# Performance work log

Hardware: AMD Instinct MI355X
Metric: run time of the kernel (lower is better)

Reference implementation:

```python
import jax, jax.numpy as jnp
import numpy as np

D_MODEL = 1024
NUM_HEADS = 16
HEAD_DIM = D_MODEL // NUM_HEADS
THETA = 10000.0
B, T = 4, 2048


def _cos_sin(seq_len, head_dim, theta):
    # [T, head_dim]: first half cos, second half sin (matches precompute_freqs_cis)
    freqs = 1.0 / theta ** (jnp.arange(0, head_dim, 2, dtype=jnp.float32) / head_dim)
    t = jnp.arange(seq_len, dtype=jnp.float32)
    angles = jnp.outer(t, freqs)  # [T, head_dim//2]
    return jnp.concatenate([jnp.cos(angles), jnp.sin(angles)], axis=-1)


def _apply_rope(x, cos_sin):
    # x: [B, H, T, Hd]; even/odd interleaved pairs rotated
    x1 = x[..., 0::2]
    x2 = x[..., 1::2]
    half = x.shape[-1] // 2
    cos = cos_sin[:, :half]  # [T, Hd//2]
    sin = cos_sin[:, half:]
    out = jnp.stack([x1 * cos - x2 * sin, x1 * sin + x2 * cos], axis=-1)
    return out.reshape(x.shape)


def setup_inputs() -> dict:
    key = jax.random.key(0)
    k1, k2, k3 = jax.random.split(key, 3)
    x = jax.random.normal(k1, (B, T, D_MODEL), dtype=jnp.float32)
    W_qkv = jax.random.normal(k2, (3 * D_MODEL, D_MODEL), dtype=jnp.float32) * (D_MODEL ** -0.5)
    W_out = jax.random.normal(k3, (D_MODEL, D_MODEL), dtype=jnp.float32) * (D_MODEL ** -0.5)
    return {"x": x, "W_qkv": W_qkv, "W_out": W_out}


def reference(x, W_qkv, W_out):
    Bsz, Tlen, _ = x.shape
    # fused QKV projection: einsum('...i,oi->...o')
    qkv = jnp.einsum('bti,oi->bto', x, W_qkv)  # [B, T, 3*d_model]
    # 'B T (nH Hs) -> B nH T Hs' with nH = 3*num_heads, then chunk along heads
    qkv = qkv.reshape(Bsz, Tlen, 3 * NUM_HEADS, HEAD_DIM).transpose(0, 2, 1, 3)
    q, k, v = jnp.split(qkv, 3, axis=1)  # each [B, nH, T, Hd]
    cos_sin = _cos_sin(Tlen, HEAD_DIM, THETA)
    q = _apply_rope(q, cos_sin)
    k = _apply_rope(k, cos_sin)
    scores = jnp.einsum('bhqd,bhkd->bhqk', q, k) / np.sqrt(HEAD_DIM).astype(np.float32)
    causal = jnp.tril(jnp.ones((Tlen, Tlen), dtype=bool))
    scores = jnp.where(causal[None, None], scores, -jnp.inf)
    attn = jax.nn.softmax(scores, axis=-1)
    o = jnp.einsum('bhqk,bhkd->bhqd', attn, v)  # [B, nH, T, Hd]
    o = o.transpose(0, 2, 1, 3).reshape(Bsz, Tlen, D_MODEL)
    return jnp.einsum('bti,oi->bto', o, W_out)
```

## Files before the change

kernel.cpp:

```cpp
#include <hip/hip_runtime.h>
#include <hip/hip_bf16.h>
#include <math.h>

constexpr int Bb  = 4;
constexpr int Tt  = 2048;
constexpr int DM  = 1024;
constexpr int NH  = 16;
constexpr int HD  = 64;
constexpr int MBT = Bb * Tt;
constexpr float LOG_THETA = 9.210340371976184f;

using bf16x8 = __attribute__((ext_vector_type(8))) short;
using f32x4  = __attribute__((ext_vector_type(4))) float;

__device__ inline short f2bf(float x) {
    __hip_bfloat16 h = __float2bfloat16(x);
    return *reinterpret_cast<short*>(&h);
}
__device__ inline float bf2f(short u) {
    __hip_bfloat16 h;
    *reinterpret_cast<short*>(&h) = u;
    return __bfloat162float(h);
}
__device__ inline unsigned int packbf2(float x) {
    short h  = f2bf(x);
    short lo = f2bf(x - bf2f(h));
    return (unsigned int)(unsigned short)h | ((unsigned int)(unsigned short)lo << 16);
}
__device__ inline void split8(float4 a, float4 b, bf16x8& H, bf16x8& L) {
    float x[8] = {a.x, a.y, a.z, a.w, b.x, b.y, b.z, b.w};
    #pragma unroll
    for (int e = 0; e < 8; ++e) {
        short h = f2bf(x[e]);
        H[e] = h;
        L[e] = f2bf(x[e] - bf2f(h));
    }
}

__global__ __launch_bounds__(256) void rope_table(float* __restrict__ tab)
{
    int i = blockIdx.x * 256 + threadIdx.x;
    int t = i >> 5, p = i & 31;
    float freq = expf(-(float)(2 * p) * (LOG_THETA / 64.0f));
    float ang  = (float)t * freq;
    tab[t * 64 + 2 * p]     = cosf(ang);
    tab[t * 64 + 2 * p + 1] = sinf(ang);
}

__global__ __launch_bounds__(256) void cast_split(
    const float* __restrict__ src, short* __restrict__ hi,
    short* __restrict__ lo, int n4)
{
    int i = blockIdx.x * 256 + threadIdx.x;
    if (i >= n4) return;
    float4 v = reinterpret_cast<const float4*>(src)[i];
    short h0 = f2bf(v.x), h1 = f2bf(v.y), h2 = f2bf(v.z), h3 = f2bf(v.w);
    short l0 = f2bf(v.x - bf2f(h0));
    short l1 = f2bf(v.y - bf2f(h1));
    short l2 = f2bf(v.z - bf2f(h2));
    short l3 = f2bf(v.w - bf2f(h3));
    reinterpret_cast<short4*>(hi)[i] = make_short4(h0, h1, h2, h3);
    reinterpret_cast<short4*>(lo)[i] = make_short4(l0, l1, l2, l3);
}

__global__ __launch_bounds__(256) void gemm_qkv_mfma(
    const short* __restrict__ Xhi, const short* __restrict__ Xlo,
    const short* __restrict__ Whi, const short* __restrict__ Wlo,
    const float* __restrict__ tab,
    float* __restrict__ Qo,
    unsigned short* __restrict__ Khi_g, unsigned short* __restrict__ Klo_g,
    unsigned short* __restrict__ Vthi_g, unsigned short* __restrict__ Vtlo_g)
{
    __shared__ __align__(16) short Ah[4096], Al[4096], Bh[4096], Bl[4096];
    const int tid = threadIdx.x;
    const int bm  = blockIdx.y * 128;
    const int bn  = blockIdx.x * 128;
    const int w   = tid >> 6, l = tid & 63;
    const int wr  = w >> 1,  wc = w & 1;

    const int r0 = tid >> 2;
    const int c0 = (tid & 3) * 8;
    const size_t ga0 = (size_t)(bm + r0) * 1024 + c0;
    const size_t ga1 = (size_t)(bm + r0 + 64) * 1024 + c0;
    const size_t gb0 = (size_t)(bn + r0) * 1024 + c0;
    const size_t gb1 = (size_t)(bn + r0 + 64) * 1024 + c0;

    f32x4 acc[4][4];
    #pragma unroll
    for (int m = 0; m < 4; ++m)
        #pragma unroll
        for (int n = 0; n < 4; ++n) acc[m][n] = (f32x4){0.f, 0.f, 0.f, 0.f};

    float4 pah0 = *(const float4*)(Xhi + ga0);
    float4 pah1 = *(const float4*)(Xhi + ga1);
    float4 pal0 = *(const float4*)(Xlo + ga0);
    float4 pal1 = *(const float4*)(Xlo + ga1);
    float4 pbh0 = *(const float4*)(Whi + gb0);
    float4 pbh1 = *(const float4*)(Whi + gb1);
    float4 pbl0 = *(const float4*)(Wlo + gb0);
    float4 pbl1 = *(const float4*)(Wlo + gb1);

    for (int k0 = 0; k0 < 1024; k0 += 32) {
        __syncthreads();
        *(float4*)&Ah[tid * 8] = pah0;  *(float4*)&Ah[(tid + 256) * 8] = pah1;
        *(float4*)&Al[tid * 8] = pal0;  *(float4*)&Al[(tid + 256) * 8] = pal1;
        *(float4*)&Bh[tid * 8] = pbh0;  *(float4*)&Bh[(tid + 256) * 8] = pbh1;
        *(float4*)&Bl[tid * 8] = pbl0;  *(float4*)&Bl[(tid + 256) * 8] = pbl1;
        int kn = (k0 + 32) & 1023;
        pah0 = *(const float4*)(Xhi + ga0 + kn);
        pah1 = *(const float4*)(Xhi + ga1 + kn);
        pal0 = *(const float4*)(Xlo + ga0 + kn);
        pal1 = *(const float4*)(Xlo + ga1 + kn);
        pbh0 = *(const float4*)(Whi + gb0 + kn);
        pbh1 = *(const float4*)(Whi + gb1 + kn);
        pbl0 = *(const float4*)(Wlo + gb0 + kn);
        pbl1 = *(const float4*)(Wlo + gb1 + kn);
        __syncthreads();

        const int fr = l & 15;
        const int fg = (l >> 4) * 8;
        bf16x8 ah[4], alo[4], bhv[4], blo[4];
        #pragma unroll
        for (int m = 0; m < 4; ++m) {
            int ro = (wr * 64 + m * 16 + fr) * 32 + fg;
            ah[m]  = *(const bf16x8*)&Ah[ro];
            alo[m] = *(const bf16x8*)&Al[ro];
        }
        #pragma unroll
        for (int n = 0; n < 4; ++n) {
            int ro = (wc * 64 + n * 16 + fr) * 32 + fg;
            bhv[n] = *(const bf16x8*)&Bh[ro];
            blo[n] = *(const bf16x8*)&Bl[ro];
        }
        #pragma unroll
        for (int m = 0; m < 4; ++m)
            #pragma unroll
            for (int n = 0; n < 4; ++n) {
                acc[m][n] = __builtin_amdgcn_mfma_f32_16x16x32_bf16(ah[m],  bhv[n], acc[m][n], 0, 0, 0);
                acc[m][n] = __builtin_amdgcn_mfma_f32_16x16x32_bf16(ah[m],  blo[n], acc[m][n], 0, 0, 0);
                acc[m][n] = __builtin_amdgcn_mfma_f32_16x16x32_bf16(alo[m], bhv[n], acc[m][n], 0, 0, 0);
            }
    }

    const int fr = l & 15, fq = l >> 4;
    #pragma unroll
    for (int m = 0; m < 4; ++m) {
        #pragma unroll
        for (int n = 0; n < 4; ++n) {
            int col  = bn + wc * 64 + n * 16 + fr;
            int sect = col >> 10;
            int cc   = col & 1023;
            int hh   = cc >> 6, d = cc & 63;
            int de   = d & 62;
            #pragma unroll
            for (int i = 0; i < 4; ++i) {
                int r  = bm + wr * 64 + m * 16 + fq * 4 + i;
                int b_ = r >> 11, t_ = r & 2047;
                float v  = acc[m][n][i];
                float vn = __shfl_xor(v, 1);
                if (sect == 2) {
                    size_t off = ((size_t)(b_ * NH + hh) * HD + d) * Tt + t_;
                    short h = f2bf(v);
                    Vthi_g[off] = (unsigned short)h;
                    Vtlo_g[off] = (unsigned short)f2bf(v - bf2f(h));
                } else {
                    float2 cssn = *(const float2*)(tab + t_ * 64 + de);
                    float outv = (d & 1) ? (vn * cssn.y + v * cssn.x)
                                         : (v * cssn.x - vn * cssn.y);
                    size_t off = ((size_t)(b_ * NH + hh) * Tt + t_) * HD + d;
                    if (sect == 0) {
                        Qo[off] = outv;
                    } else {
                        short h = f2bf(outv);
                        Khi_g[off] = (unsigned short)h;
                        Klo_g[off] = (unsigned short)f2bf(outv - bf2f(h));
                    }
                }
            }
        }
    }
}

__global__ __launch_bounds__(256) void attn_fwd_mfma(
    const float* Q,
    const unsigned short* __restrict__ Khi_g, const unsigned short* __restrict__ Klo_g,
    const unsigned short* __restrict__ Vthi_g, const unsigned short* __restrict__ Vtlo_g,
    unsigned int* Opk)
{
    __shared__ __align__(16) short Khi[4096], Klo[4096], Vthi[4096], Vtlo[4096];
    __shared__ __align__(16) unsigned int Ppk[4][16][68];

    const int tid = threadIdx.x;
    const int w   = tid >> 6;
    const int l   = tid & 63;
    const int fr  = l & 15;
    const int hi8 = l >> 4;
    const int bh  = blockIdx.y;
    const int qi  = blockIdx.x;
    const int qbase = qi * 64 + w * 16;

    bf16x8 qh[2], ql[2];
    {
        const float* qp = Q + ((size_t)bh * Tt + qbase + fr) * HD;
        #pragma unroll
        for (int s = 0; s < 2; ++s) {
            float4 a = *(const float4*)(qp + s * 32 + hi8 * 8);
            float4 b = *(const float4*)(qp + s * 32 + hi8 * 8 + 4);
            a.x *= 0.125f; a.y *= 0.125f; a.z *= 0.125f; a.w *= 0.125f;
            b.x *= 0.125f; b.y *= 0.125f; b.z *= 0.125f; b.w *= 0.125f;
            split8(a, b, qh[s], ql[s]);
        }
    }

    f32x4 acc_o[4];
    #pragma unroll
    for (int n = 0; n < 4; ++n) acc_o[n] = (f32x4){0.f, 0.f, 0.f, 0.f};
    float mreg[4] = {-INFINITY, -INFINITY, -INFINITY, -INFINITY};
    float lreg[4] = {0.f, 0.f, 0.f, 0.f};

    const int sr = tid >> 2;
    const int sc = (tid & 3) * 16;
    const unsigned short* khg = Khi_g  + ((size_t)bh * Tt + sr) * HD + sc;
    const unsigned short* klg = Klo_g  + ((size_t)bh * Tt + sr) * HD + sc;
    const unsigned short* vhg = Vthi_g + ((size_t)bh * HD + sr) * Tt + sc;
    const unsigned short* vlg = Vtlo_g + ((size_t)bh * HD + sr) * Tt + sc;

    for (int ki = 0; ki <= qi; ++ki) {
        __syncthreads();
        {
            const size_t ko = (size_t)ki * 64 * HD;
            const size_t vo = (size_t)ki * 64;
            #pragma unroll
            for (int h = 0; h < 2; ++h) {
                int off = (sc * 2 + h * 16) ^ ((sr & 7) << 4);
                *(uint4*)((char*)Khi  + sr * 128 + off) = *(const uint4*)(khg + ko + h * 8);
                *(uint4*)((char*)Klo  + sr * 128 + off) = *(const uint4*)(klg + ko + h * 8);
                *(uint4*)((char*)Vthi + sr * 128 + off) = *(const uint4*)(vhg + vo + h * 8);
                *(uint4*)((char*)Vtlo + sr * 128 + off) = *(const uint4*)(vlg + vo + h * 8);
            }
        }
        __syncthreads();

        f32x4 acc_s[4];
        #pragma unroll
        for (int n = 0; n < 4; ++n) acc_s[n] = (f32x4){0.f, 0.f, 0.f, 0.f};
        #pragma unroll
        for (int n = 0; n < 4; ++n) {
            int row = n * 16 + fr;
            const char* kh_ = (const char*)Khi + row * 128;
            const char* kl_ = (const char*)Klo + row * 128;
            #pragma unroll
            for (int s = 0; s < 2; ++s) {
                int off = (s * 64 + hi8 * 16) ^ ((row & 7) << 4);
                bf16x8 kh = *(const bf16x8*)(kh_ + off);
                bf16x8 kl = *(const bf16x8*)(kl_ + off);
                acc_s[n] = __builtin_amdgcn_mfma_f32_16x16x32_bf16(qh[s], kh, acc_s[n], 0, 0, 0);
                acc_s[n] = __builtin_amdgcn_mfma_f32_16x16x32_bf16(qh[s], kl, acc_s[n], 0, 0, 0);
                acc_s[n] = __builtin_amdgcn_mfma_f32_16x16x32_bf16(ql[s], kh, acc_s[n], 0, 0, 0);
            }
        }

        if (ki == qi) {
            #pragma unroll
            for (int n = 0; n < 4; ++n)
                #pragma unroll
                for (int i = 0; i < 4; ++i) {
                    int kc = ki * 64 + n * 16 + fr;
                    int qr = qbase + hi8 * 4 + i;
                    if (kc > qr) acc_s[n][i] = -INFINITY;
                }
        }

        float tmax[4], scl[4], ps[4][4];
        #pragma unroll
        for (int i = 0; i < 4; ++i)
            tmax[i] = fmaxf(fmaxf(acc_s[0][i], acc_s[1][i]),
                            fmaxf(acc_s[2][i], acc_s[3][i]));
        #pragma unroll
        for (int i = 0; i < 4; ++i) {
            tmax[i] = fmaxf(tmax[i], __shfl_xor(tmax[i], 1));
            tmax[i] = fmaxf(tmax[i], __shfl_xor(tmax[i], 2));
            tmax[i] = fmaxf(tmax[i], __shfl_xor(tmax[i], 4));
            tmax[i] = fmaxf(tmax[i], __shfl_xor(tmax[i], 8));
        }
        #pragma unroll
        for (int i = 0; i < 4; ++i) {
            float mn = fmaxf(mreg[i], tmax[i]);
            scl[i]  = __expf(mreg[i] - mn);
            mreg[i] = mn;
        }
        #pragma unroll
        for (int n = 0; n < 4; ++n)
            #pragma unroll
            for (int i = 0; i < 4; ++i)
                ps[n][i] = __expf(acc_s[n][i] - mreg[i]);
        #pragma unroll
        for (int i = 0; i < 4; ++i) {
            float r = ps[0][i] + ps[1][i] + ps[2][i] + ps[3][i];
            r += __shfl_xor(r, 1);
            r += __shfl_xor(r, 2);
            r += __shfl_xor(r, 4);
            r += __shfl_xor(r, 8);
            lreg[i] = lreg[i] * scl[i] + r;
        }
        #pragma unroll
        for (int n = 0; n < 4; ++n)
            #pragma unroll
            for (int i = 0; i < 4; ++i)
                acc_o[n][i] *= scl[i];

        #pragma unroll
        for (int n = 0; n < 4; ++n)
            #pragma unroll
            for (int i = 0; i < 4; ++i)
                Ppk[w][hi8 * 4 + i][n * 16 + fr] = packbf2(ps[n][i]);

        bf16x8 pah[2], pal[2];
        #pragma unroll
        for (int s = 0; s < 2; ++s) {
            const unsigned int* pr = &Ppk[w][fr][s * 32 + hi8 * 8];
            uint4 u0 = *(const uint4*)pr;
            uint4 u1 = *(const uint4*)(pr + 4);
            unsigned int uu[8] = {u0.x, u0.y, u0.z, u0.w, u1.x, u1.y, u1.z, u1.w};
            #pragma unroll
            for (int e = 0; e < 8; ++e) {
                pah[s][e] = (short)(uu[e] & 0xffffu);
                pal[s][e] = (short)(uu[e] >> 16);
            }
        }

        #pragma unroll
        for (int n = 0; n < 4; ++n) {
            int row = n * 16 + fr;
            const char* vh_ = (const char*)Vthi + row * 128;
            const char* vl_ = (const char*)Vtlo + row * 128;
            #pragma unroll
            for (int s = 0; s < 2; ++s) {
                int off = (s * 64 + hi8 * 16) ^ ((row & 7) << 4);
                bf16x8 vh = *(const bf16x8*)(vh_ + off);
                bf16x8 vl = *(const bf16x8*)(vl_ + off);
                acc_o[n] = __builtin_amdgcn_mfma_f32_16x16x32_bf16(pah[s], vh, acc_o[n], 0, 0, 0);
                acc_o[n] = __builtin_amdgcn_mfma_f32_16x16x32_bf16(pah[s], vl, acc_o[n], 0, 0, 0);
                acc_o[n] = __builtin_amdgcn_mfma_f32_16x16x32_bf16(pal[s], vh, acc_o[n], 0, 0, 0);
            }
        }
    }

    float invl[4];
    #pragma unroll
    for (int i = 0; i < 4; ++i) invl[i] = 1.0f / lreg[i];
    unsigned int* op = Opk + ((size_t)bh * Tt + qbase) * HD;
    #pragma unroll
    for (int n = 0; n < 4; ++n)
        #pragma unroll
        for (int i = 0; i < 4; ++i)
            op[(size_t)(hi8 * 4 + i) * HD + n * 16 + fr] =
                packbf2(acc_o[n][i] * invl[i]);
}

__global__ __launch_bounds__(256) void gemm_out_mfma(
    const unsigned int* __restrict__ Opk,
    const short* __restrict__ WOhi, const short* __restrict__ WOlo,
    float* __restrict__ Out)
{
    __shared__ __align__(16) short Ah[4096], Al[4096], Bh[4096], Bl[4096];
    const int tid = threadIdx.x;
    const int bm  = blockIdx.y * 128;
    const int bn  = blockIdx.x * 128;
    const int w   = tid >> 6, l = tid & 63;
    const int wr  = w >> 1,  wc = w & 1;

    const int r0 = tid >> 2;
    const int c8 = (tid & 3) * 8;
    const int rA0 = bm + r0, rA1 = bm + r0 + 64;
    const int b0 = rA0 >> 11, t0 = rA0 & 2047;
    const int b1 = rA1 >> 11, t1 = rA1 & 2047;
    const size_t gb0 = (size_t)(bn + r0) * 1024 + c8;
    const size_t gb1 = (size_t)(bn + r0 + 64) * 1024 + c8;

    f32x4 acc[4][4];
    #pragma unroll
    for (int m = 0; m < 4; ++m)
        #pragma unroll
        for (int n = 0; n < 4; ++n) acc[m][n] = (f32x4){0.f, 0.f, 0.f, 0.f};

    uint4 ua0, ua1, ua2, ua3;
    float4 pbh0, pbh1, pbl0, pbl1;
    {
        int c = c8;
        int hh = c >> 6, d = c & 63;
        size_t ia0 = ((size_t)(b0 * NH + hh) * Tt + t0) * 64 + d;
        size_t ia1 = ((size_t)(b1 * NH + hh) * Tt + t1) * 64 + d;
        ua0 = *(const uint4*)(Opk + ia0);  ua1 = *(const uint4*)(Opk + ia0 + 4);
        ua2 = *(const uint4*)(Opk + ia1);  ua3 = *(const uint4*)(Opk + ia1 + 4);
        pbh0 = *(const float4*)(WOhi + gb0);
        pbh1 = *(const float4*)(WOhi + gb1);
        pbl0 = *(const float4*)(WOlo + gb0);
        pbl1 = *(const float4*)(WOlo + gb1);
    }

    for (int k0 = 0; k0 < 1024; k0 += 32) {
        __syncthreads();
        {
            bf16x8 H, L;
            H[0] = (short)ua0.x; L[0] = (short)(ua0.x >> 16);
            H[1] = (short)ua0.y; L[1] = (short)(ua0.y >> 16);
            H[2] = (short)ua0.z; L[2] = (short)(ua0.z >> 16);
            H[3] = (short)ua0.w; L[3] = (short)(ua0.w >> 16);
            H[4] = (short)ua1.x; L[4] = (short)(ua1.x >> 16);
            H[5] = (short)ua1.y; L[5] = (short)(ua1.y >> 16);
            H[6] = (short)ua1.z; L[6] = (short)(ua1.z >> 16);
            H[7] = (short)ua1.w; L[7] = (short)(ua1.w >> 16);
            *(bf16x8*)&Ah[tid * 8] = H;  *(bf16x8*)&Al[tid * 8] = L;
            H[0] = (short)ua2.x; L[0] = (short)(ua2.x >> 16);
            H[1] = (short)ua2.y; L[1] = (short)(ua2.y >> 16);
            H[2] = (short)ua2.z; L[2] = (short)(ua2.z >> 16);
            H[3] = (short)ua2.w; L[3] = (short)(ua2.w >> 16);
            H[4] = (short)ua3.x; L[4] = (short)(ua3.x >> 16);
            H[5] = (short)ua3.y; L[5] = (short)(ua3.y >> 16);
            H[6] = (short)ua3.z; L[6] = (short)(ua3.z >> 16);
            H[7] = (short)ua3.w; L[7] = (short)(ua3.w >> 16);
            *(bf16x8*)&Ah[(tid + 256) * 8] = H;  *(bf16x8*)&Al[(tid + 256) * 8] = L;
        }
        *(float4*)&Bh[tid * 8] = pbh0;  *(float4*)&Bh[(tid + 256) * 8] = pbh1;
        *(float4*)&Bl[tid * 8] = pbl0;  *(float4*)&Bl[(tid + 256) * 8] = pbl1;

        int kn = (k0 + 32) & 1023;
        {
            int c = kn + c8;
            int hh = c >> 6, d = c & 63;
            size_t ia0 = ((size_t)(b0 * NH + hh) * Tt + t0) * 64 + d;
            size_t ia1 = ((size_t)(b1 * NH + hh) * Tt + t1) * 64 + d;
            ua0 = *(const uint4*)(Opk + ia0);  ua1 = *(const uint4*)(Opk + ia0 + 4);
            ua2 = *(const uint4*)(Opk + ia1);  ua3 = *(const uint4*)(Opk + ia1 + 4);
            pbh0 = *(const float4*)(WOhi + gb0 + kn);
            pbh1 = *(const float4*)(WOhi + gb1 + kn);
            pbl0 = *(const float4*)(WOlo + gb0 + kn);
            pbl1 = *(const float4*)(WOlo + gb1 + kn);
        }
        __syncthreads();

        const int fr = l & 15;
        const int fg = (l >> 4) * 8;
        bf16x8 ah[4], alo[4], bhv[4], blo[4];
        #pragma unroll
        for (int m = 0; m < 4; ++m) {
            int ro = (wr * 64 + m * 16 + fr) * 32 + fg;
            ah[m]  = *(const bf16x8*)&Ah[ro];
            alo[m] = *(const bf16x8*)&Al[ro];
        }
        #pragma unroll
        for (int n = 0; n < 4; ++n) {
            int ro = (wc * 64 + n * 16 + fr) * 32 + fg;
            bhv[n] = *(const bf16x8*)&Bh[ro];
            blo[n] = *(const bf16x8*)&Bl[ro];
        }
        #pragma unroll
        for (int m = 0; m < 4; ++m)
            #pragma unroll
            for (int n = 0; n < 4; ++n) {
                acc[m][n] = __builtin_amdgcn_mfma_f32_16x16x32_bf16(ah[m],  bhv[n], acc[m][n], 0, 0, 0);
                acc[m][n] = __builtin_amdgcn_mfma_f32_16x16x32_bf16(ah[m],  blo[n], acc[m][n], 0, 0, 0);
                acc[m][n] = __builtin_amdgcn_mfma_f32_16x16x32_bf16(alo[m], bhv[n], acc[m][n], 0, 0, 0);
            }
    }

    const int fr = l & 15, fq = l >> 4;
    #pragma unroll
    for (int m = 0; m < 4; ++m)
        #pragma unroll
        for (int n = 0; n < 4; ++n) {
            int col = bn + wc * 64 + n * 16 + fr;
            #pragma unroll
            for (int i = 0; i < 4; ++i) {
                int r = bm + wr * 64 + m * 16 + fq * 4 + i;
                Out[(size_t)r * 1024 + col] = acc[m][n][i];
            }
        }
}

extern "C" void kernel_launch(void* const* d_in, const int* in_sizes, int n_in,
                              void* d_out, int out_size, void* d_ws, size_t ws_size,
                              hipStream_t stream)
{
    const float* x    = (const float*)d_in[0];
    const float* wqkv = (const float*)d_in[1];
    const float* wout = (const float*)d_in[2];
    float* out = (float*)d_out;

    char* wsb = (char*)d_ws;
    float*          Qf   = (float*)(wsb);
    unsigned int*   Opk  = (unsigned int*)(wsb);
    unsigned short* Khig = (unsigned short*)(wsb + (size_t)32 * 1048576);
    unsigned short* Klog = (unsigned short*)(wsb + (size_t)48 * 1048576);
    unsigned short* Vthig= (unsigned short*)(wsb + (size_t)64 * 1048576);
    unsigned short* Vtlog= (unsigned short*)(wsb + (size_t)80 * 1048576);
    short*          Whi  = (short*)(wsb + (size_t)96  * 1048576);
    short*          Wlo  = (short*)(wsb + (size_t)102 * 1048576);
    short*          WOhi = (short*)(wsb + (size_t)108 * 1048576);
    short*          WOlo = (short*)(wsb + (size_t)110 * 1048576);
    float*          tab  = (float*)(wsb + (size_t)112 * 1048576);

    short* Xhi = (short*)d_out;
    short* Xlo = (short*)d_out + 8388608;

    rope_table<<<256, 256, 0, stream>>>(tab);
    cast_split<<<8192, 256, 0, stream>>>(x,    Xhi,  Xlo,  2097152);
    cast_split<<<3072, 256, 0, stream>>>(wqkv, Whi,  Wlo,  786432);
    cast_split<<<1024, 256, 0, stream>>>(wout, WOhi, WOlo, 262144);

    dim3 g1(24, 64);
    gemm_qkv_mfma<<<g1, 256, 0, stream>>>(Xhi, Xlo, Whi, Wlo, tab, Qf,
                                          Khig, Klog, Vthig, Vtlog);

    dim3 g2(32, 64);
    attn_fwd_mfma<<<g2, 256, 0, stream>>>(Qf, Khig, Klog, Vthig, Vtlog, Opk);

    dim3 g3(8, 64);
    gemm_out_mfma<<<g3, 256, 0, stream>>>(Opk, WOhi, WOlo, out);
}
```

Baseline: 744.2 us.

## Prefetch K/V tiles into registers, reverse causal block order, remap GEMM blocks per XCD

```diff
diff --git a/kernel.cpp b/kernel.cpp
--- a/kernel.cpp
+++ b/kernel.cpp
@@ -73,8 +73,10 @@
 {
     __shared__ __align__(16) short Ah[4096], Al[4096], Bh[4096], Bl[4096];
     const int tid = threadIdx.x;
-    const int bm  = blockIdx.y * 128;
-    const int bn  = blockIdx.x * 128;
+    const int d_  = (int)blockIdx.y * (int)gridDim.x + (int)blockIdx.x;
+    const int wid = (d_ & 7) * 192 + (d_ >> 3);
+    const int bm  = (wid / 24) * 128;
+    const int bn  = (wid % 24) * 128;
     const int w   = tid >> 6, l = tid & 63;
     const int wr  = w >> 1,  wc = w & 1;
 
@@ -196,7 +198,7 @@
     const int fr  = l & 15;
     const int hi8 = l >> 4;
     const int bh  = blockIdx.y;
-    const int qi  = blockIdx.x;
+    const int qi  = (int)gridDim.x - 1 - (int)blockIdx.x;
     const int qbase = qi * 64 + w * 16;
 
     bf16x8 qh[2], ql[2];
@@ -225,21 +227,39 @@
     const unsigned short* vhg = Vthi_g + ((size_t)bh * HD + sr) * Tt + sc;
     const unsigned short* vlg = Vtlo_g + ((size_t)bh * HD + sr) * Tt + sc;
 
+    uint4 rkh[2], rkl[2], rvh[2], rvl[2];
+    {
+        #pragma unroll
+        for (int h = 0; h < 2; ++h) {
+            rkh[h] = *(const uint4*)(khg + h * 8);
+            rkl[h] = *(const uint4*)(klg + h * 8);
+            rvh[h] = *(const uint4*)(vhg + h * 8);
+            rvl[h] = *(const uint4*)(vlg + h * 8);
+        }
+    }
+
     for (int ki = 0; ki <= qi; ++ki) {
+        #pragma unroll
+        for (int h = 0; h < 2; ++h) {
+            int off = (sc * 2 + h * 16) ^ ((sr & 7) << 4);
+            *(uint4*)((char*)Khi  + sr * 128 + off) = rkh[h];
+            *(uint4*)((char*)Klo  + sr * 128 + off) = rkl[h];
+            *(uint4*)((char*)Vthi + sr * 128 + off) = rvh[h];
+            *(uint4*)((char*)Vtlo + sr * 128 + off) = rvl[h];
+        }
         __syncthreads();
-        {
-            const size_t ko = (size_t)ki * 64 * HD;
-            const size_t vo = (size_t)ki * 64;
+
+        if (ki < qi) {
+            const size_t ko = (size_t)(ki + 1) * 64 * HD;
+            const size_t vo = (size_t)(ki + 1) * 64;
             #pragma unroll
             for (int h = 0; h < 2; ++h) {
-                int off = (sc * 2 + h * 16) ^ ((sr & 7) << 4);
-                *(uint4*)((char*)Khi  + sr * 128 + off) = *(const uint4*)(khg + ko + h * 8);
-                *(uint4*)((char*)Klo  + sr * 128 + off) = *(const uint4*)(klg + ko + h * 8);
-                *(uint4*)((char*)Vthi + sr * 128 + off) = *(const uint4*)(vhg + vo + h * 8);
-                *(uint4*)((char*)Vtlo + sr * 128 + off) = *(const uint4*)(vlg + vo + h * 8);
-            }
-        }
-        __syncthreads();
+                rkh[h] = *(const uint4*)(khg + ko + h * 8);
+                rkl[h] = *(const uint4*)(klg + ko + h * 8);
+                rvh[h] = *(const uint4*)(vhg + vo + h * 8);
+                rvl[h] = *(const uint4*)(vlg + vo + h * 8);
+            }
+        }
 
         f32x4 acc_s[4];
         #pragma unroll
@@ -344,6 +364,7 @@
                 acc_o[n] = __builtin_amdgcn_mfma_f32_16x16x32_bf16(pal[s], vh, acc_o[n], 0, 0, 0);
             }
         }
+        __syncthreads();
     }
 
     float invl[4];
@@ -365,8 +386,10 @@
 {
     __shared__ __align__(16) short Ah[4096], Al[4096], Bh[4096], Bl[4096];
     const int tid = threadIdx.x;
-    const int bm  = blockIdx.y * 128;
-    const int bn  = blockIdx.x * 128;
+    const int d_  = (int)blockIdx.y * (int)gridDim.x + (int)blockIdx.x;
+    const int wid = (d_ & 7) * 64 + (d_ >> 3);
+    const int bm  = (wid / 8) * 128;
+    const int bn  = (wid % 8) * 128;
     const int w   = tid >> 6, l = tid & 63;
     const int wr  = w >> 1,  wc = w & 1;
 
```

After: 987.7 us. 32.7% more time.

## Double attention query tile per block, reverse causal order, remap GEMM blocks for XCDs

Applied to the files above, without the earlier changes.

```diff
diff --git a/kernel.cpp b/kernel.cpp
--- a/kernel.cpp
+++ b/kernel.cpp
@@ -73,8 +73,10 @@
 {
     __shared__ __align__(16) short Ah[4096], Al[4096], Bh[4096], Bl[4096];
     const int tid = threadIdx.x;
-    const int bm  = blockIdx.y * 128;
-    const int bn  = blockIdx.x * 128;
+    const int d_  = (int)blockIdx.y * (int)gridDim.x + (int)blockIdx.x;
+    const int wid = (d_ & 7) * 192 + (d_ >> 3);
+    const int bm  = (wid / 24) * 128;
+    const int bn  = (wid % 24) * 128;
     const int w   = tid >> 6, l = tid & 63;
     const int wr  = w >> 1,  wc = w & 1;
 
@@ -196,27 +198,33 @@
     const int fr  = l & 15;
     const int hi8 = l >> 4;
     const int bh  = blockIdx.y;
-    const int qi  = blockIdx.x;
-    const int qbase = qi * 64 + w * 16;
-
-    bf16x8 qh[2], ql[2];
-    {
-        const float* qp = Q + ((size_t)bh * Tt + qbase + fr) * HD;
+    const int qi  = (int)gridDim.x - 1 - (int)blockIdx.x;
+    const int qbase = qi * 128 + w * 32;
+
+    bf16x8 qh[2][2], ql[2][2];
+    #pragma unroll
+    for (int m = 0; m < 2; ++m) {
+        const float* qp = Q + ((size_t)bh * Tt + qbase + m * 16 + fr) * HD;
         #pragma unroll
         for (int s = 0; s < 2; ++s) {
             float4 a = *(const float4*)(qp + s * 32 + hi8 * 8);
             float4 b = *(const float4*)(qp + s * 32 + hi8 * 8 + 4);
             a.x *= 0.125f; a.y *= 0.125f; a.z *= 0.125f; a.w *= 0.125f;
             b.x *= 0.125f; b.y *= 0.125f; b.z *= 0.125f; b.w *= 0.125f;
-            split8(a, b, qh[s], ql[s]);
-        }
-    }
-
-    f32x4 acc_o[4];
-    #pragma unroll
-    for (int n = 0; n < 4; ++n) acc_o[n] = (f32x4){0.f, 0.f, 0.f, 0.f};
-    float mreg[4] = {-INFINITY, -INFINITY, -INFINITY, -INFINITY};
-    float lreg[4] = {0.f, 0.f, 0.f, 0.f};
+            split8(a, b, qh[m][s], ql[m][s]);
+        }
+    }
+
+    f32x4 acc_o[2][4];
+    #pragma unroll
+    for (int m = 0; m < 2; ++m)
+        #pragma unroll
+        for (int n = 0; n < 4; ++n) acc_o[m][n] = (f32x4){0.f, 0.f, 0.f, 0.f};
+    float mreg[2][4], lreg[2][4];
+    #pragma unroll
+    for (int m = 0; m < 2; ++m)
+        #pragma unroll
+        for (int i = 0; i < 4; ++i) { mreg[m][i] = -INFINITY; lreg[m][i] = 0.f; }
 
     const int sr = tid >> 2;
     const int sc = (tid & 3) * 16;
@@ -225,7 +233,8 @@
     const unsigned short* vhg = Vthi_g + ((size_t)bh * HD + sr) * Tt + sc;
     const unsigned short* vlg = Vtlo_g + ((size_t)bh * HD + sr) * Tt + sc;
 
-    for (int ki = 0; ki <= qi; ++ki) {
+    const int ktiles = 2 * qi + 2;
+    for (int ki = 0; ki < ktiles; ++ki) {
         __syncthreads();
         {
             const size_t ko = (size_t)ki * 64 * HD;
@@ -241,9 +250,11 @@
         }
         __syncthreads();
 
-        f32x4 acc_s[4];
-        #pragma unroll
-        for (int n = 0; n < 4; ++n) acc_s[n] = (f32x4){0.f, 0.f, 0.f, 0.f};
+        f32x4 acc_s[2][4];
+        #pragma unroll
+        for (int m = 0; m < 2; ++m)
+            #pragma unroll
+            for (int n = 0; n < 4; ++n) acc_s[m][n] = (f32x4){0.f, 0.f, 0.f, 0.f};
         #pragma unroll
         for (int n = 0; n < 4; ++n) {
             int row = n * 16 + fr;
@@ -254,108 +265,119 @@
                 int off = (s * 64 + hi8 * 16) ^ ((row & 7) << 4);
                 bf16x8 kh = *(const bf16x8*)(kh_ + off);
                 bf16x8 kl = *(const bf16x8*)(kl_ + off);
-                acc_s[n] = __builtin_amdgcn_mfma_f32_16x16x32_bf16(qh[s], kh, acc_s[n], 0, 0, 0);
-                acc_s[n] = __builtin_amdgcn_mfma_f32_16x16x32_bf16(qh[s], kl, acc_s[n], 0, 0, 0);
-                acc_s[n] = __builtin_amdgcn_mfma_f32_16x16x32_bf16(ql[s], kh, acc_s[n], 0, 0, 0);
-            }
-        }
-
-        if (ki == qi) {
+                #pragma unroll
+                for (int m = 0; m < 2; ++m) {
+                    acc_s[m][n] = __builtin_amdgcn_mfma_f32_16x16x32_bf16(qh[m][s], kh, acc_s[m][n], 0, 0, 0);
+                    acc_s[m][n] = __builtin_amdgcn_mfma_f32_16x16x32_bf16(qh[m][s], kl, acc_s[m][n], 0, 0, 0);
+                    acc_s[m][n] = __builtin_amdgcn_mfma_f32_16x16x32_bf16(ql[m][s], kh, acc_s[m][n], 0, 0, 0);
+                }
+            }
+        }
+
+        if (ki >= 2 * qi) {
+            #pragma unroll
+            for (int m = 0; m < 2; ++m)
+                #pragma unroll
+                for (int n = 0; n < 4; ++n)
+                    #pragma unroll
+                    for (int i = 0; i < 4; ++i) {
+                        int kc = ki * 64 + n * 16 + fr;
+                        int qr = qbase + m * 16 + hi8 * 4 + i;
+                        if (kc > qr) acc_s[m][n][i] = -INFINITY;
+                    }
+        }
+
+        #pragma unroll
+        for (int m = 0; m < 2; ++m) {
+            float tmax[4], scl[4], ps[4][4];
+            #pragma unroll
+            for (int i = 0; i < 4; ++i)
+                tmax[i] = fmaxf(fmaxf(acc_s[m][0][i], acc_s[m][1][i]),
+                                fmaxf(acc_s[m][2][i], acc_s[m][3][i]));
+            #pragma unroll
+            for (int i = 0; i < 4; ++i) {
+                tmax[i] = fmaxf(tmax[i], __shfl_xor(tmax[i], 1));
+                tmax[i] = fmaxf(tmax[i], __shfl_xor(tmax[i], 2));
+                tmax[i] = fmaxf(tmax[i], __shfl_xor(tmax[i], 4));
+                tmax[i] = fmaxf(tmax[i], __shfl_xor(tmax[i], 8));
+            }
+            #pragma unroll
+            for (int i = 0; i < 4; ++i) {
+                float mn = fmaxf(mreg[m][i], tmax[i]);
+                scl[i]     = __expf(mreg[m][i] - mn);
+                mreg[m][i] = mn;
+            }
             #pragma unroll
             for (int n = 0; n < 4; ++n)
                 #pragma unroll
-                for (int i = 0; i < 4; ++i) {
-                    int kc = ki * 64 + n * 16 + fr;
-                    int qr = qbase + hi8 * 4 + i;
-                    if (kc > qr) acc_s[n][i] = -INFINITY;
+                for (int i = 0; i < 4; ++i)
+                    ps[n][i] = __expf(acc_s[m][n][i] - mreg[m][i]);
+            #pragma unroll
+            for (int i = 0; i < 4; ++i) {
+                float r = ps[0][i] + ps[1][i] + ps[2][i] + ps[3][i];
+                r += __shfl_xor(r, 1);
+                r += __shfl_xor(r, 2);
+                r += __shfl_xor(r, 4);
+                r += __shfl_xor(r, 8);
+                lreg[m][i] = lreg[m][i] * scl[i] + r;
+            }
+            #pragma unroll
+            for (int n = 0; n < 4; ++n)
+                #pragma unroll
+                for (int i = 0; i < 4; ++i)
+                    acc_o[m][n][i] *= scl[i];
+
+            #pragma unroll
+            for (int n = 0; n < 4; ++n)
+                #pragma unroll
+                for (int i = 0; i < 4; ++i)
+                    Ppk[w][hi8 * 4 + i][n * 16 + fr] = packbf2(ps[n][i]);
+
+            bf16x8 pah[2], pal[2];
+            #pragma unroll
+            for (int s = 0; s < 2; ++s) {
+                const unsigned int* pr = &Ppk[w][fr][s * 32 + hi8 * 8];
+                uint4 u0 = *(const uint4*)pr;
+                uint4 u1 = *(const uint4*)(pr + 4);
+                unsigned int uu[8] = {u0.x, u0.y, u0.z, u0.w, u1.x, u1.y, u1.z, u1.w};
+                #pragma unroll
+                for (int e = 0; e < 8; ++e) {
+                    pah[s][e] = (short)(uu[e] & 0xffffu);
+                    pal[s][e] = (short)(uu[e] >> 16);
                 }
-        }
-
-        float tmax[4], scl[4], ps[4][4];
-        #pragma unroll
-        for (int i = 0; i < 4; ++i)
-            tmax[i] = fmaxf(fmaxf(acc_s[0][i], acc_s[1][i]),
-                            fmaxf(acc_s[2][i], acc_s[3][i]));
-        #pragma unroll
-        for (int i = 0; i < 4; ++i) {
-            tmax[i] = fmaxf(tmax[i], __shfl_xor(tmax[i], 1));
-            tmax[i] = fmaxf(tmax[i], __shfl_xor(tmax[i], 2));
-            tmax[i] = fmaxf(tmax[i], __shfl_xor(tmax[i], 4));
-            tmax[i] = fmaxf(tmax[i], __shfl_xor(tmax[i], 8));
-        }
-        #pragma unroll
-        for (int i = 0; i < 4; ++i) {
-            float mn = fmaxf(mreg[i], tmax[i]);
-            scl[i]  = __expf(mreg[i] - mn);
-            mreg[i] = mn;
-        }
+            }
+
+            #pragma unroll
+            for (int n = 0; n < 4; ++n) {
+                int row = n * 16 + fr;
+                const char* vh_ = (const char*)Vthi + row * 128;
+                const char* vl_ = (const char*)Vtlo + row * 128;
+                #pragma unroll
+                for (int s = 0; s < 2; ++s) {
+                    int off = (s * 64 + hi8 * 16) ^ ((row & 7) << 4);
+                    bf16x8 vh = *(const bf16x8*)(vh_ + off);
+                    bf16x8 vl = *(const bf16x8*)(vl_ + off);
+                    acc_o[m][n] = __builtin_amdgcn_mfma_f32_16x16x32_bf16(pah[s], vh, acc_o[m][n], 0, 0, 0);
+                    acc_o[m][n] = __builtin_amdgcn_mfma_f32_16x16x32_bf16(pah[s], vl, acc_o[m][n], 0, 0, 0);
+                    acc_o[m][n] = __builtin_amdgcn_mfma_f32_16x16x32_bf16(pal[s], vh, acc_o[m][n], 0, 0, 0);
+                }
+            }
+        }
+    }
+
+    unsigned int* op = Opk + ((size_t)bh * Tt + qbase) * HD;
+    #pragma unroll
+    for (int m = 0; m < 2; ++m) {
+        float invl[4];
+        #pragma unroll
+        for (int i = 0; i < 4; ++i) invl[i] = 1.0f / lreg[m][i];
         #pragma unroll
         for (int n = 0; n < 4; ++n)
             #pragma unroll
             for (int i = 0; i < 4; ++i)
-                ps[n][i] = __expf(acc_s[n][i] - mreg[i]);
-        #pragma unroll
-        for (int i = 0; i < 4; ++i) {
-            float r = ps[0][i] + ps[1][i] + ps[2][i] + ps[3][i];
-            r += __shfl_xor(r, 1);
-            r += __shfl_xor(r, 2);
-            r += __shfl_xor(r, 4);
-            r += __shfl_xor(r, 8);
-            lreg[i] = lreg[i] * scl[i] + r;
-        }
-        #pragma unroll
-        for (int n = 0; n < 4; ++n)
-            #pragma unroll
-            for (int i = 0; i < 4; ++i)
-                acc_o[n][i] *= scl[i];
-
-        #pragma unroll
-        for (int n = 0; n < 4; ++n)
-            #pragma unroll
-            for (int i = 0; i < 4; ++i)
-                Ppk[w][hi8 * 4 + i][n * 16 + fr] = packbf2(ps[n][i]);
-
-        bf16x8 pah[2], pal[2];
-        #pragma unroll
-        for (int s = 0; s < 2; ++s) {
-            const unsigned int* pr = &Ppk[w][fr][s * 32 + hi8 * 8];
-            uint4 u0 = *(const uint4*)pr;
-            uint4 u1 = *(const uint4*)(pr + 4);
-            unsigned int uu[8] = {u0.x, u0.y, u0.z, u0.w, u1.x, u1.y, u1.z, u1.w};
-            #pragma unroll
-            for (int e = 0; e < 8; ++e) {
-                pah[s][e] = (short)(uu[e] & 0xffffu);
-                pal[s][e] = (short)(uu[e] >> 16);
-            }
-        }
-
-        #pragma unroll
-        for (int n = 0; n < 4; ++n) {
-            int row = n * 16 + fr;
-            const char* vh_ = (const char*)Vthi + row * 128;
-            const char* vl_ = (const char*)Vtlo + row * 128;
-            #pragma unroll
-            for (int s = 0; s < 2; ++s) {
-                int off = (s * 64 + hi8 * 16) ^ ((row & 7) << 4);
-                bf16x8 vh = *(const bf16x8*)(vh_ + off);
-                bf16x8 vl = *(const bf16x8*)(vl_ + off);
-                acc_o[n] = __builtin_amdgcn_mfma_f32_16x16x32_bf16(pah[s], vh, acc_o[n], 0, 0, 0);
-                acc_o[n] = __builtin_amdgcn_mfma_f32_16x16x32_bf16(pah[s], vl, acc_o[n], 0, 0, 0);
-                acc_o[n] = __builtin_amdgcn_mfma_f32_16x16x32_bf16(pal[s], vh, acc_o[n], 0, 0, 0);
-            }
-        }
-    }
-
-    float invl[4];
-    #pragma unroll
-    for (int i = 0; i < 4; ++i) invl[i] = 1.0f / lreg[i];
-    unsigned int* op = Opk + ((size_t)bh * Tt + qbase) * HD;
-    #pragma unroll
-    for (int n = 0; n < 4; ++n)
-        #pragma unroll
-        for (int i = 0; i < 4; ++i)
-            op[(size_t)(hi8 * 4 + i) * HD + n * 16 + fr] =
-                packbf2(acc_o[n][i] * invl[i]);
+                op[(size_t)(m * 16 + hi8 * 4 + i) * HD + n * 16 + fr] =
+                    packbf2(acc_o[m][n][i] * invl[i]);
+    }
 }
 
 __global__ __launch_bounds__(256) void gemm_out_mfma(
@@ -365,8 +387,10 @@
 {
     __shared__ __align__(16) short Ah[4096], Al[4096], Bh[4096], Bl[4096];
     const int tid = threadIdx.x;
-    const int bm  = blockIdx.y * 128;
-    const int bn  = blockIdx.x * 128;
+    const int d_  = (int)blockIdx.y * (int)gridDim.x + (int)blockIdx.x;
+    const int wid = (d_ & 7) * 64 + (d_ >> 3);
+    const int bm  = (wid / 8) * 128;
+    const int bn  = (wid % 8) * 128;
     const int w   = tid >> 6, l = tid & 63;
     const int wr  = w >> 1,  wc = w & 1;
 
@@ -513,7 +537,7 @@
     gemm_qkv_mfma<<<g1, 256, 0, stream>>>(Xhi, Xlo, Whi, Wlo, tab, Qf,
                                           Khig, Klog, Vthig, Vtlog);
 
-    dim3 g2(32, 64);
+    dim3 g2(16, 64);
     attn_fwd_mfma<<<g2, 256, 0, stream>>>(Qf, Khig, Klog, Vthig, Vtlog, Opk);
 
     dim3 g3(8, 64);
```

Measured after the change: 687.0 us. 1.08x faster.
